# Performance work log

Measured on AMD Instinct MI355X. Metric: run time of the kernel, lower is better.

## Reference

```python
import jax, jax.numpy as jnp
import numpy as np

B, N = 1, 1024
NF, EF, H, HEADS = 27, 17, 128, 4


def setup_inputs() -> dict:
    key = jax.random.key(0)
    ks = jax.random.split(key, 10)
    def w(k, shape, fan_in):
        return jax.random.normal(k, shape, jnp.float32) / np.sqrt(fan_in).astype(np.float32)
    return {
        "node_features": jax.random.normal(ks[0], (B, N, NF), jnp.float32),
        # node encoder: Linear(NF,H) -> ReLU -> Linear(H,H)  (dropout = eval/no-op)
        "enc_w1": w(ks[1], (NF, H), NF), "enc_b1": jnp.zeros((H,), jnp.float32),
        "enc_w2": w(ks[2], (H, H), H),  "enc_b2": jnp.zeros((H,), jnp.float32),
        # MHA in-projection (packed q|k|v as in torch). out_proj omitted: the
        # attention *output* is dead code (only averaged weights are returned).
        "in_proj_w": w(ks[3], (H, 3 * H), H), "in_proj_b": jnp.zeros((3 * H,), jnp.float32),
        # edge feature predictor: Linear(2H,H) -> ReLU -> Linear(H,EF)
        "pred_w1": w(ks[4], (2 * H, H), 2 * H), "pred_b1": jnp.zeros((H,), jnp.float32),
        "pred_w2": w(ks[5], (H, EF), H),        "pred_b2": jnp.zeros((EF,), jnp.float32),
        # edge classifier: Linear(2H,H//2) -> ReLU -> Linear(H//2,1) -> Sigmoid
        "cls_w1": w(ks[6], (2 * H, H // 2), 2 * H), "cls_b1": jnp.zeros((H // 2,), jnp.float32),
        "cls_w2": w(ks[7], (H // 2, 1), H // 2),    "cls_b2": jnp.zeros((1,), jnp.float32),
    }


def reference(node_features, enc_w1, enc_b1, enc_w2, enc_b2,
              in_proj_w, in_proj_b,
              pred_w1, pred_b1, pred_w2, pred_b2,
              cls_w1, cls_b1, cls_w2, cls_b2):
    # node encoder (dropout in eval mode = identity)
    enc = jax.nn.relu(node_features @ enc_w1 + enc_b1) @ enc_w2 + enc_b2  # [B,N,H]
    hd = H // HEADS
    # self-attention weights, averaged over heads (torch MHA default)
    q = (enc @ in_proj_w[:, :H] + in_proj_b[:H]).reshape(B, N, HEADS, hd)
    k = (enc @ in_proj_w[:, H:2 * H] + in_proj_b[H:2 * H]).reshape(B, N, HEADS, hd)
    scores = jnp.einsum('bqhd,bkhd->bhqk', q, k) / jnp.asarray(np.sqrt(hd), jnp.float32)
    attention_weights = jax.nn.softmax(scores, axis=-1).mean(axis=1)  # [B,N,N]
    # pairwise concat([src, tgt]) @ W == src @ W[:H] + tgt @ W[H:] (fused, no 2H concat)
    sa_p = enc @ pred_w1[:H]   # [B,N,H]
    sb_p = enc @ pred_w1[H:]
    hp = jax.nn.relu(sa_p[:, :, None, :] + sb_p[:, None, :, :] + pred_b1)  # [B,N,N,H]
    predicted_edge_features = hp @ pred_w2 + pred_b2                        # [B,N,N,EF]
    sa_c = enc @ cls_w1[:H]
    sb_c = enc @ cls_w1[H:]
    hc = jax.nn.relu(sa_c[:, :, None, :] + sb_c[:, None, :, :] + cls_b1)   # [B,N,N,H//2]
    edge_probabilities = jax.nn.sigmoid((hc @ cls_w2 + cls_b2)[..., 0])    # [B,N,N]
    return attention_weights, edge_probabilities, predicted_edge_features
```

## Files before the change

kernel.cpp:

```cpp
#include <hip/hip_runtime.h>
#include <hip/hip_bf16.h>

#define N 1024
#define NF 27
#define EF 17
#define H 128
#define HEADS 4
#define HD 32

typedef __attribute__((ext_vector_type(8))) short bf16x8;
typedef __attribute__((ext_vector_type(16))) float f32x16;

__device__ __forceinline__ short f2bf(float x) {
  return __builtin_bit_cast(short, __float2bfloat16(x));
}
__device__ __forceinline__ unsigned pk2bf(float a, float b) {
  const unsigned lo = (unsigned short)f2bf(a);
  const unsigned hi = (unsigned short)f2bf(b);
  return lo | (hi << 16);
}

__global__ __launch_bounds__(256) void k_front(
    const float* __restrict__ nf,
    const float* __restrict__ ew1, const float* __restrict__ eb1,
    const float* __restrict__ ew2, const float* __restrict__ eb2,
    const float* __restrict__ ipw, const float* __restrict__ ipb,
    const float* __restrict__ pw1, const float* __restrict__ pb1,
    const float* __restrict__ cw1, const float* __restrict__ pw2,
    float* __restrict__ q, float* __restrict__ kkT,
    float* __restrict__ sa_pb, float* __restrict__ sb_ps,
    float* __restrict__ sa_c, float* __restrict__ sb_cT,
    unsigned short* __restrict__ w2f)
{
  const int t = threadIdx.x;
  if (blockIdx.x == 256) {
    if (t < 64) {
      const int lane = t, col = lane & 31, hsel = lane >> 5;
      for (int kc = 0; kc < 8; ++kc)
        for (int e = 0; e < 8; ++e) {
          const int k = kc * 16 + hsel * 8 + e;
          w2f[(kc * 64 + lane) * 8 + e] =
              (unsigned short)((col < EF) ? (unsigned short)f2bf(pw2[k * EF + col]) : 0);
        }
    }
    return;
  }

  __shared__ float s_nf[4 * NF];
  __shared__ float s_h1[4][H];
  __shared__ float s_e[4][H];
  const int i0 = blockIdx.x * 4;
  if (t < 4 * NF) s_nf[t] = nf[i0 * NF + t];
  __syncthreads();

  {
    const int half = t >> 7, c = t & 127;
    #pragma unroll
    for (int rr = 0; rr < 2; ++rr) {
      const int row = rr * 2 + half;
      float h = eb1[c];
      #pragma unroll
      for (int f = 0; f < NF; ++f) h = fmaf(s_nf[row * NF + f], ew1[f * H + c], h);
      s_h1[row][c] = fmaxf(h, 0.f);
    }
  }
  __syncthreads();
  {
    const int half = t >> 7, c = t & 127;
    #pragma unroll
    for (int rr = 0; rr < 2; ++rr) {
      const int row = rr * 2 + half;
      float e = eb2[c];
      #pragma unroll 8
      for (int k = 0; k < H; ++k) e = fmaf(s_h1[row][k], ew2[k * H + c], e);
      s_e[row][c] = e;
    }
  }
  __syncthreads();

  for (int c = t; c < 640; c += 256) {
    float a0, a1, a2, a3;
    if (c < 256) {
      a0 = a1 = a2 = a3 = ipb[c];
      const float* wcol = ipw + c;
      #pragma unroll 8
      for (int k = 0; k < H; ++k) {
        const float w = wcol[k * 384];
        a0 = fmaf(s_e[0][k], w, a0); a1 = fmaf(s_e[1][k], w, a1);
        a2 = fmaf(s_e[2][k], w, a2); a3 = fmaf(s_e[3][k], w, a3);
      }
      if (c < 128) {
        q[i0 * H + c] = a0; q[(i0 + 1) * H + c] = a1;
        q[(i0 + 2) * H + c] = a2; q[(i0 + 3) * H + c] = a3;
      } else {
        float* kp = kkT + (c - 128) * N + i0;
        kp[0] = a0; kp[1] = a1; kp[2] = a2; kp[3] = a3;
      }
    } else if (c < 512) {
      const int cc = (c < 384) ? (c - 256) : (c - 384);
      const float* wcol = (c < 384) ? (pw1 + cc) : (pw1 + 128 * H + cc);
      a0 = a1 = a2 = a3 = 0.f;
      #pragma unroll 8
      for (int k = 0; k < H; ++k) {
        const float w = wcol[k * H];
        a0 = fmaf(s_e[0][k], w, a0); a1 = fmaf(s_e[1][k], w, a1);
        a2 = fmaf(s_e[2][k], w, a2); a3 = fmaf(s_e[3][k], w, a3);
      }
      if (c < 384) {
        const float bb = pb1[cc];
        sa_pb[i0 * H + cc] = a0 + bb;
        sa_pb[(i0 + 1) * H + cc] = a1 + bb;
        sa_pb[(i0 + 2) * H + cc] = a2 + bb;
        sa_pb[(i0 + 3) * H + cc] = a3 + bb;
      } else {
        const int J = i0 >> 5, jl = i0 & 31;
        const int kc = cc >> 4, hs = (cc >> 3) & 1, hf = (cc >> 2) & 1, pos = cc & 3;
        const int base = ((J * 32 + kc * 4 + hs * 2 + hf) * 32) * 4 + pos;
        sb_ps[base + (jl + 0) * 4] = a0;
        sb_ps[base + (jl + 1) * 4] = a1;
        sb_ps[base + (jl + 2) * 4] = a2;
        sb_ps[base + (jl + 3) * 4] = a3;
      }
    } else {
      const int cc = (c < 576) ? (c - 512) : (c - 576);
      const float* wcol = (c < 576) ? (cw1 + cc) : (cw1 + 128 * 64 + cc);
      a0 = a1 = a2 = a3 = 0.f;
      #pragma unroll 8
      for (int k = 0; k < H; ++k) {
        const float w = wcol[k * 64];
        a0 = fmaf(s_e[0][k], w, a0); a1 = fmaf(s_e[1][k], w, a1);
        a2 = fmaf(s_e[2][k], w, a2); a3 = fmaf(s_e[3][k], w, a3);
      }
      if (c < 576) {
        sa_c[i0 * 64 + cc] = a0; sa_c[(i0 + 1) * 64 + cc] = a1;
        sa_c[(i0 + 2) * 64 + cc] = a2; sa_c[(i0 + 3) * 64 + cc] = a3;
      } else {
        float* sp = sb_cT + cc * N + i0;
        sp[0] = a0; sp[1] = a1; sp[2] = a2; sp[3] = a3;
      }
    }
  }
}

#define PAIR_BLOCKS 2048
#define ATTN_BLOCKS 512
#define CLS_BLOCKS  512

__global__ __launch_bounds__(256) void k_main(
    const float* __restrict__ sa_pb, const float* __restrict__ sb_ps,
    const unsigned short* __restrict__ w2f, const float* __restrict__ pb2,
    const float* __restrict__ q, const float* __restrict__ kkT,
    const float* __restrict__ sa_c, const float* __restrict__ sb_cT,
    const float* __restrict__ cb1, const float* __restrict__ cw2, const float* __restrict__ cb2,
    float* __restrict__ out0, float* __restrict__ out1, float* __restrict__ out2)
{
  __shared__ float4 s_buf[1536];
  const int t = threadIdx.x;
  const int b = blockIdx.x;

  if (b < PAIR_BLOCKS) {
    float4* s_sb = s_buf;
    float*  s_ap = (float*)(s_buf + 1024);

    const int lane = t & 63, wid = t >> 6;
    const int It = b >> 5;
    const int J  = b & 31;
    const int i0 = It * 16;
    const int col = lane & 31, hsel = lane >> 5;

    const float4* g_sb = ((const float4*)sb_ps) + J * 1024;
    #pragma unroll
    for (int c = t; c < 1024; c += 256) s_sb[c] = g_sb[c];
    const float4* g_ap = (const float4*)(sa_pb + i0 * H);
    ((float4*)s_ap)[t] = g_ap[t];
    ((float4*)s_ap)[t + 256] = g_ap[t + 256];

    const bf16x8* w2f8 = (const bf16x8*)w2f;
    bf16x8 bfrag[8];
    #pragma unroll
    for (int kc = 0; kc < 8; ++kc) bfrag[kc] = w2f8[kc * 64 + lane];
    const float pb2c = (col < EF) ? pb2[col] : 0.f;
    __syncthreads();

    const int ia = wid * 4;
    f32x16 acc0, acc1, acc2, acc3;
    #pragma unroll
    for (int r = 0; r < 16; ++r) { acc0[r] = 0.f; acc1[r] = 0.f; acc2[r] = 0.f; acc3[r] = 0.f; }

    #pragma unroll
    for (int kc = 0; kc < 8; ++kc) {
      const int cl = (kc * 4 + hsel * 2) * 32 + col;
      const float4 v0 = s_sb[cl];
      const float4 v1 = s_sb[cl + 32];
      const int ko = kc * 16 + hsel * 8;
      const float* p0 = s_ap + (ia + 0) * H + ko;
      const float* p1 = s_ap + (ia + 1) * H + ko;
      const float* p2 = s_ap + (ia + 2) * H + ko;
      const float* p3 = s_ap + (ia + 3) * H + ko;
      const float4 c00 = *(const float4*)p0, c01 = *(const float4*)(p0 + 4);
      const float4 c10 = *(const float4*)p1, c11 = *(const float4*)(p1 + 4);
      const float4 c20 = *(const float4*)p2, c21 = *(const float4*)(p2 + 4);
      const float4 c30 = *(const float4*)p3, c31 = *(const float4*)(p3 + 4);
      union { bf16x8 v8; unsigned u[4]; } u0, u1, u2, u3;
      u0.u[0] = pk2bf(fmaxf(c00.x + v0.x, 0.f), fmaxf(c00.y + v0.y, 0.f));
      u0.u[1] = pk2bf(fmaxf(c00.z + v0.z, 0.f), fmaxf(c00.w + v0.w, 0.f));
      u0.u[2] = pk2bf(fmaxf(c01.x + v1.x, 0.f), fmaxf(c01.y + v1.y, 0.f));
      u0.u[3] = pk2bf(fmaxf(c01.z + v1.z, 0.f), fmaxf(c01.w + v1.w, 0.f));
      u1.u[0] = pk2bf(fmaxf(c10.x + v0.x, 0.f), fmaxf(c10.y + v0.y, 0.f));
      u1.u[1] = pk2bf(fmaxf(c10.z + v0.z, 0.f), fmaxf(c10.w + v0.w, 0.f));
      u1.u[2] = pk2bf(fmaxf(c11.x + v1.x, 0.f), fmaxf(c11.y + v1.y, 0.f));
      u1.u[3] = pk2bf(fmaxf(c11.z + v1.z, 0.f), fmaxf(c11.w + v1.w, 0.f));
      u2.u[0] = pk2bf(fmaxf(c20.x + v0.x, 0.f), fmaxf(c20.y + v0.y, 0.f));
      u2.u[1] = pk2bf(fmaxf(c20.z + v0.z, 0.f), fmaxf(c20.w + v0.w, 0.f));
      u2.u[2] = pk2bf(fmaxf(c21.x + v1.x, 0.f), fmaxf(c21.y + v1.y, 0.f));
      u2.u[3] = pk2bf(fmaxf(c21.z + v1.z, 0.f), fmaxf(c21.w + v1.w, 0.f));
      u3.u[0] = pk2bf(fmaxf(c30.x + v0.x, 0.f), fmaxf(c30.y + v0.y, 0.f));
      u3.u[1] = pk2bf(fmaxf(c30.z + v0.z, 0.f), fmaxf(c30.w + v0.w, 0.f));
      u3.u[2] = pk2bf(fmaxf(c31.x + v1.x, 0.f), fmaxf(c31.y + v1.y, 0.f));
      u3.u[3] = pk2bf(fmaxf(c31.z + v1.z, 0.f), fmaxf(c31.w + v1.w, 0.f));
      acc0 = __builtin_amdgcn_mfma_f32_32x32x16_bf16(u0.v8, bfrag[kc], acc0, 0, 0, 0);
      acc1 = __builtin_amdgcn_mfma_f32_32x32x16_bf16(u1.v8, bfrag[kc], acc1, 0, 0, 0);
      acc2 = __builtin_amdgcn_mfma_f32_32x32x16_bf16(u2.v8, bfrag[kc], acc2, 0, 0, 0);
      acc3 = __builtin_amdgcn_mfma_f32_32x32x16_bf16(u3.v8, bfrag[kc], acc3, 0, 0, 0);
    }

    if (col < EF) {
      const int jbase = J * 32 + 4 * hsel;
      float* o0 = out2 + ((size_t)(i0 + ia + 0) * N + jbase) * EF + col;
      float* o1 = out2 + ((size_t)(i0 + ia + 1) * N + jbase) * EF + col;
      float* o2 = out2 + ((size_t)(i0 + ia + 2) * N + jbase) * EF + col;
      float* o3 = out2 + ((size_t)(i0 + ia + 3) * N + jbase) * EF + col;
      #pragma unroll
      for (int r = 0; r < 16; ++r) {
        const int off = ((r & 3) + 8 * (r >> 2)) * EF;
        o0[off] = acc0[r] + pb2c;
        o1[off] = acc1[r] + pb2c;
        o2[off] = acc2[r] + pb2c;
        o3[off] = acc3[r] + pb2c;
      }
    }
    return;
  }

  if (b < PAIR_BLOCKS + ATTN_BLOCKS) {
    float (*s_q)[H] = (float(*)[H])s_buf;
    float (*s_redm)[4] = (float(*)[4])((float*)s_buf + 2 * H);
    float (*s_reds)[4] = (float(*)[4])((float*)s_buf + 2 * H + 32);

    const int i0 = (b - PAIR_BLOCKS) * 2;
    const int w = t >> 6, lane = t & 63;
    s_q[t >> 7][t & 127] = q[(i0 + (t >> 7)) * H + (t & 127)];
    __syncthreads();

    const float scale = 0.17677669529663687f;
    const float4* kT4 = (const float4*)kkT;
    float4 sc[2][4];

    #pragma unroll
    for (int h = 0; h < HEADS; ++h) {
      float4 a0 = {0.f, 0.f, 0.f, 0.f}, a1 = {0.f, 0.f, 0.f, 0.f};
      #pragma unroll 8
      for (int d = 0; d < HD; ++d) {
        const float4 kv = kT4[(h * HD + d) * 256 + t];
        const float q0 = s_q[0][h * HD + d], q1 = s_q[1][h * HD + d];
        a0.x = fmaf(q0, kv.x, a0.x); a0.y = fmaf(q0, kv.y, a0.y);
        a0.z = fmaf(q0, kv.z, a0.z); a0.w = fmaf(q0, kv.w, a0.w);
        a1.x = fmaf(q1, kv.x, a1.x); a1.y = fmaf(q1, kv.y, a1.y);
        a1.z = fmaf(q1, kv.z, a1.z); a1.w = fmaf(q1, kv.w, a1.w);
      }
      sc[0][h].x = a0.x * scale; sc[0][h].y = a0.y * scale;
      sc[0][h].z = a0.z * scale; sc[0][h].w = a0.w * scale;
      sc[1][h].x = a1.x * scale; sc[1][h].y = a1.y * scale;
      sc[1][h].z = a1.z * scale; sc[1][h].w = a1.w * scale;
    }

    float m[2][4];
    #pragma unroll
    for (int ti = 0; ti < 2; ++ti)
      #pragma unroll
      for (int h = 0; h < HEADS; ++h) {
        float mm = fmaxf(fmaxf(sc[ti][h].x, sc[ti][h].y), fmaxf(sc[ti][h].z, sc[ti][h].w));
        for (int off = 32; off; off >>= 1) mm = fmaxf(mm, __shfl_xor(mm, off));
        if (lane == 0) s_redm[ti * 4 + h][w] = mm;
      }
    __syncthreads();
    #pragma unroll
    for (int ti = 0; ti < 2; ++ti)
      #pragma unroll
      for (int h = 0; h < HEADS; ++h) {
        const int idx = ti * 4 + h;
        m[ti][h] = fmaxf(fmaxf(s_redm[idx][0], s_redm[idx][1]),
                         fmaxf(s_redm[idx][2], s_redm[idx][3]));
      }

    float inv[2][4];
    #pragma unroll
    for (int ti = 0; ti < 2; ++ti)
      #pragma unroll
      for (int h = 0; h < HEADS; ++h) {
        sc[ti][h].x = __expf(sc[ti][h].x - m[ti][h]);
        sc[ti][h].y = __expf(sc[ti][h].y - m[ti][h]);
        sc[ti][h].z = __expf(sc[ti][h].z - m[ti][h]);
        sc[ti][h].w = __expf(sc[ti][h].w - m[ti][h]);
        float s = sc[ti][h].x + sc[ti][h].y + sc[ti][h].z + sc[ti][h].w;
        for (int off = 32; off; off >>= 1) s += __shfl_xor(s, off);
        if (lane == 0) s_reds[ti * 4 + h][w] = s;
      }
    __syncthreads();
    #pragma unroll
    for (int ti = 0; ti < 2; ++ti)
      #pragma unroll
      for (int h = 0; h < HEADS; ++h) {
        const int idx = ti * 4 + h;
        inv[ti][h] = 0.25f / (s_reds[idx][0] + s_reds[idx][1] + s_reds[idx][2] + s_reds[idx][3]);
      }

    #pragma unroll
    for (int ti = 0; ti < 2; ++ti) {
      float4 o;
      o.x = sc[ti][0].x * inv[ti][0] + sc[ti][1].x * inv[ti][1] +
            sc[ti][2].x * inv[ti][2] + sc[ti][3].x * inv[ti][3];
      o.y = sc[ti][0].y * inv[ti][0] + sc[ti][1].y * inv[ti][1] +
            sc[ti][2].y * inv[ti][2] + sc[ti][3].y * inv[ti][3];
      o.z = sc[ti][0].z * inv[ti][0] + sc[ti][1].z * inv[ti][1] +
            sc[ti][2].z * inv[ti][2] + sc[ti][3].z * inv[ti][3];
      o.w = sc[ti][0].w * inv[ti][0] + sc[ti][1].w * inv[ti][1] +
            sc[ti][2].w * inv[ti][2] + sc[ti][3].w * inv[ti][3];
      ((float4*)(out0 + (size_t)(i0 + ti) * N))[t] = o;
    }
    return;
  }

  {
    float (*s_ac)[64] = (float(*)[64])s_buf;
    const int i0 = (b - PAIR_BLOCKS - ATTN_BLOCKS) * 2;
    if (t < 128)
      s_ac[t >> 6][t & 63] = sa_c[(i0 + (t >> 6)) * 64 + (t & 63)] + cb1[t & 63];
    __syncthreads();

    const float4* sbc4 = (const float4*)sb_cT;
    float4 ac0 = {0.f, 0.f, 0.f, 0.f}, ac1 = {0.f, 0.f, 0.f, 0.f};
    #pragma unroll 4
    for (int k = 0; k < 64; ++k) {
      const float4 sb = sbc4[k * 256 + t];
      const float a0 = s_ac[0][k], a1 = s_ac[1][k];
      const float we = cw2[k];
      ac0.x = fmaf(fmaxf(a0 + sb.x, 0.f), we, ac0.x);
      ac0.y = fmaf(fmaxf(a0 + sb.y, 0.f), we, ac0.y);
      ac0.z = fmaf(fmaxf(a0 + sb.z, 0.f), we, ac0.z);
      ac0.w = fmaf(fmaxf(a0 + sb.w, 0.f), we, ac0.w);
      ac1.x = fmaf(fmaxf(a1 + sb.x, 0.f), we, ac1.x);
      ac1.y = fmaf(fmaxf(a1 + sb.y, 0.f), we, ac1.y);
      ac1.z = fmaf(fmaxf(a1 + sb.z, 0.f), we, ac1.z);
      ac1.w = fmaf(fmaxf(a1 + sb.w, 0.f), we, ac1.w);
    }
    const float cb = cb2[0];
    float4 o0, o1;
    o0.x = 1.f / (1.f + __expf(-(ac0.x + cb)));
    o0.y = 1.f / (1.f + __expf(-(ac0.y + cb)));
    o0.z = 1.f / (1.f + __expf(-(ac0.z + cb)));
    o0.w = 1.f / (1.f + __expf(-(ac0.w + cb)));
    o1.x = 1.f / (1.f + __expf(-(ac1.x + cb)));
    o1.y = 1.f / (1.f + __expf(-(ac1.y + cb)));
    o1.z = 1.f / (1.f + __expf(-(ac1.z + cb)));
    o1.w = 1.f / (1.f + __expf(-(ac1.w + cb)));
    ((float4*)(out1 + (size_t)i0 * N))[t] = o0;
    ((float4*)(out1 + (size_t)(i0 + 1) * N))[t] = o1;
  }
}

extern "C" void kernel_launch(void* const* d_in, const int* in_sizes, int n_in,
                              void* d_out, int out_size, void* d_ws, size_t ws_size,
                              hipStream_t stream) {
  const float* nf  = (const float*)d_in[0];
  const float* ew1 = (const float*)d_in[1];
  const float* eb1 = (const float*)d_in[2];
  const float* ew2 = (const float*)d_in[3];
  const float* eb2 = (const float*)d_in[4];
  const float* ipw = (const float*)d_in[5];
  const float* ipb = (const float*)d_in[6];
  const float* pw1 = (const float*)d_in[7];
  const float* pb1 = (const float*)d_in[8];
  const float* pw2 = (const float*)d_in[9];
  const float* pb2 = (const float*)d_in[10];
  const float* cw1 = (const float*)d_in[11];
  const float* cb1 = (const float*)d_in[12];
  const float* cw2 = (const float*)d_in[13];
  const float* cb2 = (const float*)d_in[14];

  float* ws = (float*)d_ws;
  float* q     = ws + 131072;
  float* kkT   = ws + 262144;
  float* sa_pb = ws + 393216;
  float* sb_ps = ws + 524288;
  float* sa_c  = ws + 655360;
  float* sb_cT = ws + 720896;
  unsigned short* w2f = (unsigned short*)(ws + 786432);

  float* out0 = (float*)d_out;
  float* out1 = out0 + N * N;
  float* out2 = out0 + 2 * N * N;

  k_front<<<257, 256, 0, stream>>>(nf, ew1, eb1, ew2, eb2, ipw, ipb, pw1, pb1, cw1, pw2,
                                   q, kkT, sa_pb, sb_ps, sa_c, sb_cT, w2f);
  k_main<<<PAIR_BLOCKS + ATTN_BLOCKS + CLS_BLOCKS, 256, 0, stream>>>(
      sa_pb, sb_ps, w2f, pb2, q, kkT, sa_c, sb_cT, cb1, cw2, cb2, out0, out1, out2);
}
```

Baseline: 72.64 us.

## Halve pair-block row tile and interleave pair, attention and classifier blocks

The edge-feature pair blocks now cover 8 rows instead of 16, so there are 4096 of them, each wave doing 2 MFMA chains instead of 4, and shared memory shrinks. Blocks are interleaved in groups of 10 (8 pair, 1 attention, 1 classifier) so the different workloads run at the same time instead of in separate phases. The aim is better occupancy and a balanced mix of memory-bound and compute-bound blocks across CUs. The cost is that each sb tile is reloaded twice as often per output row, raising LDS fill traffic per unit of work.

```diff
diff --git a/kernel.cpp b/kernel.cpp
--- a/kernel.cpp
+++ b/kernel.cpp
@@ -142,9 +142,7 @@
   }
 }
 
-#define PAIR_BLOCKS 2048
-#define ATTN_BLOCKS 512
-#define CLS_BLOCKS  512
+#define MAIN_BLOCKS 5120
 
 __global__ __launch_bounds__(256) void k_main(
     const float* __restrict__ sa_pb, const float* __restrict__ sb_ps,
@@ -154,26 +152,25 @@
     const float* __restrict__ cb1, const float* __restrict__ cw2, const float* __restrict__ cb2,
     float* __restrict__ out0, float* __restrict__ out1, float* __restrict__ out2)
 {
-  __shared__ float4 s_buf[1536];
+  __shared__ float4 s_buf[1280];
   const int t = threadIdx.x;
-  const int b = blockIdx.x;
-
-  if (b < PAIR_BLOCKS) {
+  const int g = blockIdx.x / 10, r = blockIdx.x % 10;
+
+  if (r < 8) {
+    const int pb = g * 8 + r;
     float4* s_sb = s_buf;
     float*  s_ap = (float*)(s_buf + 1024);
 
     const int lane = t & 63, wid = t >> 6;
-    const int It = b >> 5;
-    const int J  = b & 31;
-    const int i0 = It * 16;
+    const int It = pb >> 5;
+    const int J  = pb & 31;
+    const int i0 = It * 8;
     const int col = lane & 31, hsel = lane >> 5;
 
     const float4* g_sb = ((const float4*)sb_ps) + J * 1024;
     #pragma unroll
     for (int c = t; c < 1024; c += 256) s_sb[c] = g_sb[c];
-    const float4* g_ap = (const float4*)(sa_pb + i0 * H);
-    ((float4*)s_ap)[t] = g_ap[t];
-    ((float4*)s_ap)[t + 256] = g_ap[t + 256];
+    ((float4*)s_ap)[t] = ((const float4*)(sa_pb + i0 * H))[t];
 
     const bf16x8* w2f8 = (const bf16x8*)w2f;
     bf16x8 bfrag[8];
@@ -182,72 +179,55 @@
     const float pb2c = (col < EF) ? pb2[col] : 0.f;
     __syncthreads();
 
-    const int ia = wid * 4;
-    f32x16 acc0, acc1, acc2, acc3;
-    #pragma unroll
-    for (int r = 0; r < 16; ++r) { acc0[r] = 0.f; acc1[r] = 0.f; acc2[r] = 0.f; acc3[r] = 0.f; }
+    const int ia = wid * 2, ib = ia + 1;
+    f32x16 accA, accB;
+    #pragma unroll
+    for (int rr = 0; rr < 16; ++rr) { accA[rr] = 0.f; accB[rr] = 0.f; }
 
     #pragma unroll
     for (int kc = 0; kc < 8; ++kc) {
       const int cl = (kc * 4 + hsel * 2) * 32 + col;
       const float4 v0 = s_sb[cl];
       const float4 v1 = s_sb[cl + 32];
-      const int ko = kc * 16 + hsel * 8;
-      const float* p0 = s_ap + (ia + 0) * H + ko;
-      const float* p1 = s_ap + (ia + 1) * H + ko;
-      const float* p2 = s_ap + (ia + 2) * H + ko;
-      const float* p3 = s_ap + (ia + 3) * H + ko;
-      const float4 c00 = *(const float4*)p0, c01 = *(const float4*)(p0 + 4);
-      const float4 c10 = *(const float4*)p1, c11 = *(const float4*)(p1 + 4);
-      const float4 c20 = *(const float4*)p2, c21 = *(const float4*)(p2 + 4);
-      const float4 c30 = *(const float4*)p3, c31 = *(const float4*)(p3 + 4);
-      union { bf16x8 v8; unsigned u[4]; } u0, u1, u2, u3;
-      u0.u[0] = pk2bf(fmaxf(c00.x + v0.x, 0.f), fmaxf(c00.y + v0.y, 0.f));
-      u0.u[1] = pk2bf(fmaxf(c00.z + v0.z, 0.f), fmaxf(c00.w + v0.w, 0.f));
-      u0.u[2] = pk2bf(fmaxf(c01.x + v1.x, 0.f), fmaxf(c01.y + v1.y, 0.f));
-      u0.u[3] = pk2bf(fmaxf(c01.z + v1.z, 0.f), fmaxf(c01.w + v1.w, 0.f));
-      u1.u[0] = pk2bf(fmaxf(c10.x + v0.x, 0.f), fmaxf(c10.y + v0.y, 0.f));
-      u1.u[1] = pk2bf(fmaxf(c10.z + v0.z, 0.f), fmaxf(c10.w + v0.w, 0.f));
-      u1.u[2] = pk2bf(fmaxf(c11.x + v1.x, 0.f), fmaxf(c11.y + v1.y, 0.f));
-      u1.u[3] = pk2bf(fmaxf(c11.z + v1.z, 0.f), fmaxf(c11.w + v1.w, 0.f));
-      u2.u[0] = pk2bf(fmaxf(c20.x + v0.x, 0.f), fmaxf(c20.y + v0.y, 0.f));
-      u2.u[1] = pk2bf(fmaxf(c20.z + v0.z, 0.f), fmaxf(c20.w + v0.w, 0.f));
-      u2.u[2] = pk2bf(fmaxf(c21.x + v1.x, 0.f), fmaxf(c21.y + v1.y, 0.f));
-      u2.u[3] = pk2bf(fmaxf(c21.z + v1.z, 0.f), fmaxf(c21.w + v1.w, 0.f));
-      u3.u[0] = pk2bf(fmaxf(c30.x + v0.x, 0.f), fmaxf(c30.y + v0.y, 0.f));
-      u3.u[1] = pk2bf(fmaxf(c30.z + v0.z, 0.f), fmaxf(c30.w + v0.w, 0.f));
-      u3.u[2] = pk2bf(fmaxf(c31.x + v1.x, 0.f), fmaxf(c31.y + v1.y, 0.f));
-      u3.u[3] = pk2bf(fmaxf(c31.z + v1.z, 0.f), fmaxf(c31.w + v1.w, 0.f));
-      acc0 = __builtin_amdgcn_mfma_f32_32x32x16_bf16(u0.v8, bfrag[kc], acc0, 0, 0, 0);
-      acc1 = __builtin_amdgcn_mfma_f32_32x32x16_bf16(u1.v8, bfrag[kc], acc1, 0, 0, 0);
-      acc2 = __builtin_amdgcn_mfma_f32_32x32x16_bf16(u2.v8, bfrag[kc], acc2, 0, 0, 0);
-      acc3 = __builtin_amdgcn_mfma_f32_32x32x16_bf16(u3.v8, bfrag[kc], acc3, 0, 0, 0);
+      const float* apA = s_ap + ia * H + kc * 16 + hsel * 8;
+      const float* apB = s_ap + ib * H + kc * 16 + hsel * 8;
+      const float4 a0 = *(const float4*)apA;
+      const float4 a1 = *(const float4*)(apA + 4);
+      const float4 b0 = *(const float4*)apB;
+      const float4 b1 = *(const float4*)(apB + 4);
+      union { bf16x8 v8; unsigned u[4]; } uA, uB;
+      uA.u[0] = pk2bf(fmaxf(a0.x + v0.x, 0.f), fmaxf(a0.y + v0.y, 0.f));
+      uA.u[1] = pk2bf(fmaxf(a0.z + v0.z, 0.f), fmaxf(a0.w + v0.w, 0.f));
+      uA.u[2] = pk2bf(fmaxf(a1.x + v1.x, 0.f), fmaxf(a1.y + v1.y, 0.f));
+      uA.u[3] = pk2bf(fmaxf(a1.z + v1.z, 0.f), fmaxf(a1.w + v1.w, 0.f));
+      uB.u[0] = pk2bf(fmaxf(b0.x + v0.x, 0.f), fmaxf(b0.y + v0.y, 0.f));
+      uB.u[1] = pk2bf(fmaxf(b0.z + v0.z, 0.f), fmaxf(b0.w + v0.w, 0.f));
+      uB.u[2] = pk2bf(fmaxf(b1.x + v1.x, 0.f), fmaxf(b1.y + v1.y, 0.f));
+      uB.u[3] = pk2bf(fmaxf(b1.z + v1.z, 0.f), fmaxf(b1.w + v1.w, 0.f));
+      accA = __builtin_amdgcn_mfma_f32_32x32x16_bf16(uA.v8, bfrag[kc], accA, 0, 0, 0);
+      accB = __builtin_amdgcn_mfma_f32_32x32x16_bf16(uB.v8, bfrag[kc], accB, 0, 0, 0);
     }
 
     if (col < EF) {
       const int jbase = J * 32 + 4 * hsel;
-      float* o0 = out2 + ((size_t)(i0 + ia + 0) * N + jbase) * EF + col;
-      float* o1 = out2 + ((size_t)(i0 + ia + 1) * N + jbase) * EF + col;
-      float* o2 = out2 + ((size_t)(i0 + ia + 2) * N + jbase) * EF + col;
-      float* o3 = out2 + ((size_t)(i0 + ia + 3) * N + jbase) * EF + col;
-      #pragma unroll
-      for (int r = 0; r < 16; ++r) {
-        const int off = ((r & 3) + 8 * (r >> 2)) * EF;
-        o0[off] = acc0[r] + pb2c;
-        o1[off] = acc1[r] + pb2c;
-        o2[off] = acc2[r] + pb2c;
-        o3[off] = acc3[r] + pb2c;
+      float* oA = out2 + ((size_t)(i0 + ia) * N + jbase) * EF + col;
+      float* oB = out2 + ((size_t)(i0 + ib) * N + jbase) * EF + col;
+      #pragma unroll
+      for (int rr = 0; rr < 16; ++rr) {
+        const int off = ((rr & 3) + 8 * (rr >> 2)) * EF;
+        oA[off] = accA[rr] + pb2c;
+        oB[off] = accB[rr] + pb2c;
       }
     }
     return;
   }
 
-  if (b < PAIR_BLOCKS + ATTN_BLOCKS) {
+  if (r == 8) {
     float (*s_q)[H] = (float(*)[H])s_buf;
     float (*s_redm)[4] = (float(*)[4])((float*)s_buf + 2 * H);
     float (*s_reds)[4] = (float(*)[4])((float*)s_buf + 2 * H + 32);
 
-    const int i0 = (b - PAIR_BLOCKS) * 2;
+    const int i0 = g * 2;
     const int w = t >> 6, lane = t & 63;
     s_q[t >> 7][t & 127] = q[(i0 + (t >> 7)) * H + (t & 127)];
     __syncthreads();
@@ -333,7 +313,7 @@
 
   {
     float (*s_ac)[64] = (float(*)[64])s_buf;
-    const int i0 = (b - PAIR_BLOCKS - ATTN_BLOCKS) * 2;
+    const int i0 = g * 2;
     if (t < 128)
       s_ac[t >> 6][t & 63] = sa_c[(i0 + (t >> 6)) * 64 + (t & 63)] + cb1[t & 63];
     __syncthreads();
@@ -403,6 +383,6 @@
 
   k_front<<<257, 256, 0, stream>>>(nf, ew1, eb1, ew2, eb2, ipw, ipb, pw1, pb1, cw1, pw2,
                                    q, kkT, sa_pb, sb_ps, sa_c, sb_cT, w2f);
-  k_main<<<PAIR_BLOCKS + ATTN_BLOCKS + CLS_BLOCKS, 256, 0, stream>>>(
+  k_main<<<MAIN_BLOCKS, 256, 0, stream>>>(
       sa_pb, sb_ps, w2f, pb2, q, kkT, sa_c, sb_cT, cb1, cw2, cb2, out0, out1, out2);
 }
```

Result: slower. 78.49 us (+8.1%).
